# Kernel optimization log

Measured on AMD Instinct MI355X. Metric: run time of the kernel, lower is better.

## Reference

```python
import jax, jax.numpy as jnp
import numpy as np

NUM_VOXELS = 1_000_000
N_POINTS = 1_500_000
TOTAL_PROP_PTS = 1_000_000
NUM_PROPOSALS = 2048
IN_CH = 134  # 3 + 3 + 128
M = 16       # backbone output width
BATCH = 8


def setup_inputs() -> dict:
    key = jax.random.key(0)
    k1, k2, k3, k4, k5, k6 = jax.random.split(key, 6)
    voxel_feats = jax.random.normal(k1, (NUM_VOXELS, IN_CH), dtype=jnp.float32)
    W = jax.random.normal(k2, (IN_CH, M), dtype=jnp.float32) * 0.05
    p2v_map = jax.random.randint(k3, (N_POINTS,), 0, NUM_VOXELS, dtype=jnp.int64)
    # column 0: proposal id (unused), column 1: point index into pt_feats
    col1 = jax.random.randint(k4, (TOTAL_PROP_PTS,), 0, N_POINTS, dtype=jnp.int64)
    gt_proposals_idx = jnp.stack([jnp.zeros_like(col1), col1], axis=1)
    interior = jnp.sort(jax.random.randint(k5, (NUM_PROPOSALS - 1,), 0, TOTAL_PROP_PTS, dtype=jnp.int64))
    gt_proposals_offset = jnp.concatenate([
        jnp.zeros((1,), jnp.int64), interior,
        jnp.full((1,), TOTAL_PROP_PTS, jnp.int64)])
    # column 0 is the batch (scene) id
    locs_scaled = jax.random.randint(k6, (N_POINTS, 4), 0, BATCH, dtype=jnp.int32)
    return {
        'voxel_feats': voxel_feats,
        'W': W,
        'p2v_map': p2v_map,
        'gt_proposals_idx': gt_proposals_idx,
        'gt_proposals_offset': gt_proposals_offset,
        'locs_scaled': locs_scaled,
    }


def reference(voxel_feats, W, p2v_map, gt_proposals_idx, gt_proposals_offset, locs_scaled):
    # Stand-in for the Minkowski sparse backbone: pointwise projection + ReLU, 134 -> 16.
    feats = jax.nn.relu(voxel_feats @ W)                 # (V, 16)
    pt_feats = feats[p2v_map]                            # (N, 16) voxel->point gather

    P = gt_proposals_offset.shape[0] - 1
    point_idx = gt_proposals_idx[:, 1]                   # (T,)
    T = point_idx.shape[0]

    # CSR offsets -> segment ids (replaces the Python loop over proposals)
    seg_ids = jnp.searchsorted(gt_proposals_offset, jnp.arange(T), side='right') - 1

    gathered = pt_feats[point_idx]                       # (T, 16) ragged gather
    sums = jax.ops.segment_sum(gathered, seg_ids, num_segments=P)
    counts = jax.ops.segment_sum(jnp.ones((T,), feats.dtype), seg_ids, num_segments=P)
    proposal_feats = sums / jnp.maximum(counts, 1.0)[:, None]   # (P, 16) segment mean

    batch_idxs = locs_scaled[:, 0]                       # (N,) scene ids
    proposals_batchId = batch_idxs[point_idx][gt_proposals_offset[:-1]]  # (P,)
    proposal_objectness_scores = jnp.ones((P,), dtype=bool)
    return proposal_feats, proposals_batchId, proposal_objectness_scores
```

## Files before the change

kernel.cpp:

```cpp
#include <hip/hip_runtime.h>

#define NUM_VOXELS     1000000
#define N_POINTS       1500000
#define TOTAL_PROP_PTS 1000000
#define NUM_PROPOSALS  2048
#define IN_CH          134
#define M_OUT          16

#define G1 ((NUM_VOXELS + 255) / 256)
#define GV ((TOTAL_PROP_PTS + 255) / 256)

__global__ __launch_bounds__(256, 4) void k_gemm_relu_vt(
    const float* __restrict__ A, const float* __restrict__ W,
    const int* __restrict__ p2v, const int* __restrict__ prop_idx,
    float* __restrict__ feats, int* __restrict__ vt)
{
    if (blockIdx.x >= G1) {
        const int t = (blockIdx.x - G1) * 256 + threadIdx.x;
        if (t < TOTAL_PROP_PTS) {
            const int2* pidx2 = (const int2*)prop_idx;
            vt[t] = p2v[pidx2[t].y];
        }
        return;
    }

    __shared__ float lds[4][64 * 33];
    const int wave = threadIdx.x >> 6;
    const int lane = threadIdx.x & 63;
    const int v0   = blockIdx.x * 256 + wave * 64;
    if (v0 >= NUM_VOXELS) return;

    float* chunk = lds[wave];

    const float* myrow = A + (size_t)(v0 + lane) * IN_CH;
    const float2 tl0 = *(const float2*)(myrow + 128);
    const float2 tl1 = *(const float2*)(myrow + 130);
    const float2 tl2 = *(const float2*)(myrow + 132);

    const int srow = lane >> 4;
    const int scol = (lane & 15) * 2;
    const float* sbase = A + (size_t)(v0 + srow) * IN_CH + scol;

    float2 buf[16];
#pragma unroll
    for (int j = 0; j < 16; ++j)
        buf[j] = *(const float2*)(sbase + (size_t)j * 4 * IN_CH);

    float acc[M_OUT];
#pragma unroll
    for (int c = 0; c < M_OUT; ++c) acc[c] = 0.f;

#pragma unroll
    for (int cidx = 0; cidx < 4; ++cidx) {
        const int kc = cidx * 32;
#pragma unroll
        for (int j = 0; j < 16; ++j) {
            const int row = j * 4 + srow;
            *(float2*)&chunk[row * 33 + scol] = buf[j];
        }
        if (cidx < 3) {
            const float* nb = sbase + kc + 32;
#pragma unroll
            for (int j = 0; j < 16; ++j)
                buf[j] = *(const float2*)(nb + (size_t)j * 4 * IN_CH);
        }
        const float* wbase = W + kc * M_OUT;
#pragma unroll
        for (int kk = 0; kk < 32; ++kk) {
            const float a = chunk[lane * 33 + kk];
            const float* wr = wbase + kk * M_OUT;
#pragma unroll
            for (int c = 0; c < M_OUT; ++c) acc[c] = fmaf(a, wr[c], acc[c]);
        }
    }
    {
        const float* wr = W + 128 * M_OUT;
#pragma unroll
        for (int c = 0; c < M_OUT; ++c) {
            float v = fmaf(tl0.x, wr[0 * M_OUT + c], acc[c]);
            v = fmaf(tl0.y, wr[1 * M_OUT + c], v);
            v = fmaf(tl1.x, wr[2 * M_OUT + c], v);
            v = fmaf(tl1.y, wr[3 * M_OUT + c], v);
            v = fmaf(tl2.x, wr[4 * M_OUT + c], v);
            acc[c] = fmaf(tl2.y, wr[5 * M_OUT + c], v);
        }
    }
    float4* orow = (float4*)(feats + (size_t)(v0 + lane) * M_OUT);
#pragma unroll
    for (int q = 0; q < 4; ++q) {
        float4 o;
        o.x = fmaxf(acc[q * 4 + 0], 0.f);
        o.y = fmaxf(acc[q * 4 + 1], 0.f);
        o.z = fmaxf(acc[q * 4 + 2], 0.f);
        o.w = fmaxf(acc[q * 4 + 3], 0.f);
        orow[q] = o;
    }
}

__global__ __launch_bounds__(256) void k_propmean(
    const float* __restrict__ feats,
    const int*   __restrict__ vt,
    const int*   __restrict__ prop_idx,
    const int*   __restrict__ offsets,
    const int*   __restrict__ locs,
    float*       __restrict__ out)
{
    const int s   = blockIdx.x;
    const int tid = threadIdx.x;
    const int t0  = offsets[s];
    const int t1  = offsets[s + 1];
    const int g   = tid >> 2;
    const int q   = tid & 3;

    float a0 = 0.f, a1 = 0.f, a2 = 0.f, a3 = 0.f;

    int t = t0 + g;
    int v = (t < t1) ? vt[t] : -1;

    for (int base = t0; base < t1; base += 64) {
        const int tn = t + 64;
        const int vn = (tn < t1) ? vt[tn] : -1;

        if (v >= 0) {
            const float4 f = *(const float4*)(feats + (size_t)v * M_OUT + q * 4);
            a0 += f.x; a1 += f.y; a2 += f.z; a3 += f.w;
        }
        v = vn; t = tn;
    }

#pragma unroll
    for (int off = 4; off < 64; off <<= 1) {
        a0 += __shfl_down(a0, off, 64);
        a1 += __shfl_down(a1, off, 64);
        a2 += __shfl_down(a2, off, 64);
        a3 += __shfl_down(a3, off, 64);
    }

    __shared__ float red[4][4][4];
    const int lane = tid & 63, wv = tid >> 6;
    if (lane < 4) {
        red[wv][lane][0] = a0; red[wv][lane][1] = a1;
        red[wv][lane][2] = a2; red[wv][lane][3] = a3;
    }
    __syncthreads();

    if (tid < M_OUT) {
        const float sum = red[0][tid >> 2][tid & 3] + red[1][tid >> 2][tid & 3]
                        + red[2][tid >> 2][tid & 3] + red[3][tid >> 2][tid & 3];
        const float cnt = (float)(t1 - t0);
        out[s * M_OUT + tid] = sum / fmaxf(cnt, 1.f);
    }
    if (tid == 0) {
        const int p = prop_idx[2 * t0 + 1];
        out[NUM_PROPOSALS * M_OUT + s]                 = (float)locs[4 * p];
        out[NUM_PROPOSALS * M_OUT + NUM_PROPOSALS + s] = 1.0f;
    }
}

extern "C" void kernel_launch(void* const* d_in, const int* in_sizes, int n_in,
                              void* d_out, int out_size, void* d_ws, size_t ws_size,
                              hipStream_t stream)
{
    const float* A    = (const float*)d_in[0];
    const float* W    = (const float*)d_in[1];
    const int*   p2v  = (const int*)  d_in[2];
    const int*   pidx = (const int*)  d_in[3];
    const int*   offs = (const int*)  d_in[4];
    const int*   locs = (const int*)  d_in[5];
    float*       out  = (float*)      d_out;

    float* feats = (float*)d_ws;
    int*   vt    = (int*)((char*)d_ws + (size_t)64 * 1024 * 1024);

    k_gemm_relu_vt<<<G1 + GV, 256, 0, stream>>>(A, W, p2v, pidx, feats, vt);
    k_propmean<<<NUM_PROPOSALS, 256, 0, stream>>>(feats, vt, pidx, offs, locs, out);
}
```

Measured before the change: 777.9 us.

## Compute backbone features only for voxels referenced by proposal points

Adds two prep kernels. The first builds the proposal-point-to-voxel map and clears a per-voxel flag array. The second marks every voxel that a proposal point reaches. The GEMM+ReLU kernel then exits waves that have no flagged voxels and skips loading rows and storing outputs for unflagged voxels, which cuts DRAM reads of the 134-wide input. This costs two extra launches and a scattered byte write, and the inner k-loop unroll drops to 8.

Result: no change. 781.1 us (+0.4%).

```diff
diff --git a/kernel.cpp b/kernel.cpp
--- a/kernel.cpp
+++ b/kernel.cpp
@@ -8,34 +8,51 @@
 #define M_OUT          16
 
 #define G1 ((NUM_VOXELS + 255) / 256)
-#define GV ((TOTAL_PROP_PTS + 255) / 256)
-
-__global__ __launch_bounds__(256, 4) void k_gemm_relu_vt(
+#define GP ((TOTAL_PROP_PTS + 255) / 256)
+
+
+__global__ __launch_bounds__(256) void k_prep1(
+    const int* __restrict__ p2v, const int* __restrict__ prop_idx,
+    int* __restrict__ vt, uint4* __restrict__ flag16)
+{
+    const int t = blockIdx.x * 256 + threadIdx.x;
+    if (t < NUM_VOXELS / 16)
+        flag16[t] = make_uint4(0u, 0u, 0u, 0u);
+    if (t < TOTAL_PROP_PTS) {
+        const int2* pidx2 = (const int2*)prop_idx;
+        vt[t] = p2v[pidx2[t].y];
+    }
+}
+
+__global__ __launch_bounds__(256) void k_prep2(
+    const int* __restrict__ vt, unsigned char* __restrict__ flag)
+{
+    const int t = blockIdx.x * 256 + threadIdx.x;
+    if (t < TOTAL_PROP_PTS) flag[vt[t]] = 1;
+}
+
+__global__ __launch_bounds__(256, 4) void k_gemm_relu(
     const float* __restrict__ A, const float* __restrict__ W,
-    const int* __restrict__ p2v, const int* __restrict__ prop_idx,
-    float* __restrict__ feats, int* __restrict__ vt)
-{
-    if (blockIdx.x >= G1) {
-        const int t = (blockIdx.x - G1) * 256 + threadIdx.x;
-        if (t < TOTAL_PROP_PTS) {
-            const int2* pidx2 = (const int2*)prop_idx;
-            vt[t] = p2v[pidx2[t].y];
-        }
-        return;
-    }
-
+    const unsigned char* __restrict__ flag,
+    float* __restrict__ feats)
+{
     __shared__ float lds[4][64 * 33];
     const int wave = threadIdx.x >> 6;
     const int lane = threadIdx.x & 63;
     const int v0   = blockIdx.x * 256 + wave * 64;
     if (v0 >= NUM_VOXELS) return;
 
+    const int myflag = flag[v0 + lane];
+    const unsigned long long fm = __ballot(myflag != 0);
+    if (fm == 0ull) return;
+
     float* chunk = lds[wave];
+    const float2 z2 = make_float2(0.f, 0.f);
 
     const float* myrow = A + (size_t)(v0 + lane) * IN_CH;
-    const float2 tl0 = *(const float2*)(myrow + 128);
-    const float2 tl1 = *(const float2*)(myrow + 130);
-    const float2 tl2 = *(const float2*)(myrow + 132);
+    const float2 tl0 = myflag ? *(const float2*)(myrow + 128) : z2;
+    const float2 tl1 = myflag ? *(const float2*)(myrow + 130) : z2;
+    const float2 tl2 = myflag ? *(const float2*)(myrow + 132) : z2;
 
     const int srow = lane >> 4;
     const int scol = (lane & 15) * 2;
@@ -43,8 +60,10 @@
 
     float2 buf[16];
 #pragma unroll
-    for (int j = 0; j < 16; ++j)
-        buf[j] = *(const float2*)(sbase + (size_t)j * 4 * IN_CH);
+    for (int j = 0; j < 16; ++j) {
+        const bool want = (fm >> (j * 4 + srow)) & 1ull;
+        buf[j] = want ? *(const float2*)(sbase + (size_t)j * 4 * IN_CH) : z2;
+    }
 
     float acc[M_OUT];
 #pragma unroll
@@ -61,11 +80,13 @@
         if (cidx < 3) {
             const float* nb = sbase + kc + 32;
 #pragma unroll
-            for (int j = 0; j < 16; ++j)
-                buf[j] = *(const float2*)(nb + (size_t)j * 4 * IN_CH);
+            for (int j = 0; j < 16; ++j) {
+                const bool want = (fm >> (j * 4 + srow)) & 1ull;
+                buf[j] = want ? *(const float2*)(nb + (size_t)j * 4 * IN_CH) : z2;
+            }
         }
         const float* wbase = W + kc * M_OUT;
-#pragma unroll
+#pragma unroll 8
         for (int kk = 0; kk < 32; ++kk) {
             const float a = chunk[lane * 33 + kk];
             const float* wr = wbase + kk * M_OUT;
@@ -85,15 +106,17 @@
             acc[c] = fmaf(tl2.y, wr[5 * M_OUT + c], v);
         }
     }
-    float4* orow = (float4*)(feats + (size_t)(v0 + lane) * M_OUT);
-#pragma unroll
-    for (int q = 0; q < 4; ++q) {
-        float4 o;
-        o.x = fmaxf(acc[q * 4 + 0], 0.f);
-        o.y = fmaxf(acc[q * 4 + 1], 0.f);
-        o.z = fmaxf(acc[q * 4 + 2], 0.f);
-        o.w = fmaxf(acc[q * 4 + 3], 0.f);
-        orow[q] = o;
+    if (myflag) {
+        float4* orow = (float4*)(feats + (size_t)(v0 + lane) * M_OUT);
+#pragma unroll
+        for (int q = 0; q < 4; ++q) {
+            float4 o;
+            o.x = fmaxf(acc[q * 4 + 0], 0.f);
+            o.y = fmaxf(acc[q * 4 + 1], 0.f);
+            o.z = fmaxf(acc[q * 4 + 2], 0.f);
+            o.w = fmaxf(acc[q * 4 + 3], 0.f);
+            orow[q] = o;
+        }
     }
 }
 
@@ -169,9 +192,12 @@
     const int*   locs = (const int*)  d_in[5];
     float*       out  = (float*)      d_out;
 
-    float* feats = (float*)d_ws;
-    int*   vt    = (int*)((char*)d_ws + (size_t)64 * 1024 * 1024);
-
-    k_gemm_relu_vt<<<G1 + GV, 256, 0, stream>>>(A, W, p2v, pidx, feats, vt);
+    float*         feats = (float*)d_ws;
+    int*           vt    = (int*)((char*)d_ws + (size_t)64 * 1024 * 1024);
+    unsigned char* flag  = (unsigned char*)d_ws + (size_t)68 * 1024 * 1024;
+
+    k_prep1<<<GP, 256, 0, stream>>>(p2v, pidx, vt, (uint4*)flag);
+    k_prep2<<<GP, 256, 0, stream>>>(vt, flag);
+    k_gemm_relu<<<G1, 256, 0, stream>>>(A, W, flag, feats);
     k_propmean<<<NUM_PROPOSALS, 256, 0, stream>>>(feats, vt, pidx, offs, locs, out);
 }
```
